# Kernel optimization log

Hardware: AMD Instinct MI355X
Metric: run time of the kernel (lower is better)

Reference implementation:

```python
import jax, jax.numpy as jnp
import numpy as np


def setup_inputs() -> dict:
    key = jax.random.key(0)
    pred = jax.random.normal(key, (16, 4, 768, 768), dtype=jnp.float32)
    return {"pred": pred}


def _largest_cc(mask):
    """Largest 4-connected component of a 2D boolean mask, as float32 0/1.

    Equivalent to scipy.ndimage.label (default 4-connectivity) followed by
    keeping the largest label. Uses min-label flood propagation: each
    foreground pixel starts with its raster index; iterated neighbor-min
    converges so every pixel holds its component's minimum pixel index
    (the 'root'). Ties in size resolve to the smallest root, which matches
    scipy's label-order tie-breaking (labels assigned in raster order).
    """
    H, W = mask.shape
    HW = H * W
    idx = jnp.arange(HW, dtype=jnp.int32).reshape(H, W)
    BIG = jnp.int32(HW)  # sentinel for background
    lbl0 = jnp.where(mask, idx, BIG)

    def body(carry):
        lbl, _ = carry
        p = jnp.pad(lbl, 1, constant_values=HW)
        nb = jnp.minimum(jnp.minimum(p[:-2, 1:-1], p[2:, 1:-1]),
                         jnp.minimum(p[1:-1, :-2], p[1:-1, 2:]))
        new = jnp.where(mask, jnp.minimum(lbl, nb), BIG)
        return new, jnp.any(new != lbl)

    lbl, _ = jax.lax.while_loop(lambda c: c[1], body, (lbl0, jnp.any(mask)))

    # component sizes keyed by root pixel index; background bucket = HW
    sizes = jax.ops.segment_sum(mask.ravel().astype(jnp.int32), lbl.ravel(),
                                num_segments=HW + 1)
    sizes = sizes.at[HW].set(0)
    root = jnp.argmax(sizes).astype(jnp.int32)
    return ((lbl == root) & mask).astype(jnp.float32)


def reference(pred):
    B, C, H, W = pred.shape
    labels = jnp.argmax(pred, axis=1)  # [B, H, W]
    cls = jnp.arange(1, C, dtype=labels.dtype)
    masks = labels[:, None, :, :] == cls[None, :, None, None]  # [B, C-1, H, W]
    comp = jax.vmap(_largest_cc)(masks.reshape(-1, H, W)).reshape(B, C - 1, H, W)
    bg = 1.0 - jnp.clip(comp.sum(axis=1), 0.0, 1.0)  # channel 0
    return jnp.concatenate([bg[:, None], comp], axis=1)
```

## Files before the change

### kernel.cpp

```cpp
#include <hip/hip_runtime.h>
#include <stdint.h>

#define BB 16
#define CC 4
#define HH 768
#define WW 768
#define HW (HH * WW)
#define NPIX (BB * HW)
#define NIMG (BB * (CC - 1))
#define BEST_STRIDE 16

#define SH 16
#define SW 64
#define SPIX (SH * SW)
#define SX (WW / SW)
#define SY (HH / SH)
#define SPI (SX * SY)
#define WPB 4
#define CCL_TPB (WPB * 64)

typedef unsigned long long ull;


__device__ __forceinline__ int find_root(int* P, int i) {
    int p = P[i];
    while (p != i) {
        int gp = P[p];
        P[i] = gp;
        i = p;
        p = gp;
    }
    return i;
}

__device__ __forceinline__ void merge(int* P, int a, int b) {
    a = find_root(P, a);
    b = find_root(P, b);
    while (a != b) {
        if (a < b) { int t = a; a = b; b = t; }
        int old = atomicCAS(&P[a], a, b);
        if (old == a) return;
        a = find_root(P, old);
        b = find_root(P, b);
    }
}


__device__ __forceinline__ int lfind(int* P, int i) {
    int p = P[i];
    while (p != i) {
        int gp = P[p];
        P[i] = gp;
        i = p;
        p = gp;
    }
    return i;
}

__device__ __forceinline__ void lmerge(int* P, int a, int b) {
    a = lfind(P, a);
    b = lfind(P, b);
    while (a != b) {
        if (a < b) { int t = a; a = b; b = t; }
        int old = atomicCAS(&P[a], a, b);
        if (old == a) return;
        a = lfind(P, old);
        b = lfind(P, b);
    }
}

__device__ __forceinline__ ull umax64(ull a, ull b) { return a > b ? a : b; }

__device__ __forceinline__ void lds_fence() {
    asm volatile("s_waitcnt lgkmcnt(0)" ::: "memory");
    __builtin_amdgcn_sched_barrier(0);
}


__global__ __launch_bounds__(CCL_TPB) void k_strip_ccl(
        const float* __restrict__ pred,
        uint8_t* __restrict__ labels,
        int* __restrict__ parent,
        uint32_t* __restrict__ counts,
        ull* __restrict__ best) {
    __shared__ __align__(16) int sp_all[WPB][SPIX];
    __shared__ __align__(16) uint8_t slab_all[WPB][SPIX];

    if (blockIdx.x == 0) {
        for (int i = threadIdx.x; i < NIMG * BEST_STRIDE; i += CCL_TPB) best[i] = 0ull;
    }

    const int tid = (int)threadIdx.x;
    const int w = tid >> 6;
    const int lane = tid & 63;
    int* sp = sp_all[w];
    uint8_t* slab = slab_all[w];

    const int gs = blockIdx.x * WPB + w;
    const int img = gs / SPI;
    const int s = gs % SPI;
    const int tr = (s / SX) * SH;
    const int tc = (s % SX) * SW;
    const float* pb = pred + (size_t)img * CC * HW;
    const int imgbase = img * HW;

    for (int it = 0; it < 4; ++it) {
        int li = it * 256 + lane * 4;
        int gi = (tr + (li >> 6)) * WW + tc + (li & 63);
        float4 v0 = *(const float4*)&pb[gi];
        float4 v1 = *(const float4*)&pb[gi + HW];
        float4 v2 = *(const float4*)&pb[gi + 2 * HW];
        float4 v3 = *(const float4*)&pb[gi + 3 * HW];
        const float* a0 = &v0.x; const float* a1 = &v1.x;
        const float* a2 = &v2.x; const float* a3 = &v3.x;
        uchar4 lout;
        uint8_t* lj = &lout.x;
        #pragma unroll
        for (int j = 0; j < 4; ++j) {
            int lab = 0;
            float bv = a0[j];
            if (a1[j] > bv) { bv = a1[j]; lab = 1; }
            if (a2[j] > bv) { bv = a2[j]; lab = 2; }
            if (a3[j] > bv) { bv = a3[j]; lab = 3; }
            lj[j] = (uint8_t)lab;
        }
        *(uchar4*)&slab[li] = lout;
        *(uchar4*)&labels[imgbase + gi] = lout;
    }
    lds_fence();

    {
        int prevLab = 0, prevV = 0;
        #pragma unroll 1
        for (int r = 0; r < SH; ++r) {
            int li = (r << 6) + lane;
            int lab = slab[li];
            int labL = __shfl_up(lab, 1, 64);
            bool isStart = lab && (lane == 0 || labL != lab);
            ull mask = __ballot(isStart);
            int v = li;
            if (lab) {
                ull mle = mask & (~0ull >> (63 - lane));
                v = (r << 6) + (63 - __clzll(mle));
            }
            sp[li] = v;
            lds_fence();
            int labUL = __shfl_up(prevLab, 1, 64);
            if (r > 0 && lab && prevLab == lab) {
                if (lane == 0 || !(labL == lab && labUL == lab))
                    lmerge(sp, v, prevV);
            }
            prevLab = lab;
            prevV = v;
        }
    }
    lds_fence();

    #pragma unroll 1
    for (int r = 0; r < SH; ++r) {
        int li = (r << 6) + lane;
        int lab = slab[li];
        int labL = __shfl_up(lab, 1, 64);
        bool isStart = lab && (lane == 0 || labL != lab);
        bool isEnd = lab && (lane == 63 || (int)slab[li + 1] != lab);
        ull endmask = __ballot(isEnd);
        if (lab) {
            int p = sp[li] & 0xFFFF;
            if (p != li) {
                int q0 = sp[p] & 0xFFFF;
                while (q0 != p) { p = q0; q0 = sp[p] & 0xFFFF; }
                sp[li] = p;
            }
            if (isStart) {
                ull mge = endmask & (~0ull << lane);
                int epos = __ffsll((long long)mge) - 1;
                int runlen = epos - lane + 1;
                atomicAdd((unsigned int*)&sp[p], (unsigned int)runlen << 16);
            }
        }
    }
    lds_fence();

    for (int it = 0; it < 4; ++it) {
        int li = it * 256 + lane * 4;
        int gi = imgbase + (tr + (li >> 6)) * WW + tc + (li & 63);
        uchar4 lv = *(const uchar4*)&slab[li];
        int4 sv = *(const int4*)&sp[li];
        const uint8_t* lj = &lv.x;
        const int* sj = &sv.x;
        int4 pout; uint4 cout;
        int* pj = &pout.x; uint32_t* cj = &cout.x;
        #pragma unroll
        for (int j = 0; j < 4; ++j) {
            int root = sj[j] & 0xFFFF;
            if (lj[j]) {
                pj[j] = imgbase + (tr + (root >> 6)) * WW + tc + (root & 63);
                cj[j] = (root == li + j) ? ((uint32_t)sj[j] >> 16) : 0u;
            } else {
                pj[j] = -1;
                cj[j] = 0u;
            }
        }
        *(int4*)&parent[gi] = pout;
        *(uint4*)&counts[gi] = cout;
    }
}

#define VED ((SX - 1) * HH)
#define HED ((SY - 1) * WW)
#define EPI (VED + HED)
__global__ void k_border_merge(const uint8_t* __restrict__ labels, int* parent) {
    int t = blockIdx.x * blockDim.x + threadIdx.x;
    if (t >= BB * EPI) return;
    int img = t / EPI;
    int e = t % EPI;
    int a, b;
    if (e < VED) {
        int j = e / HH, r = e % HH;
        int c = (j + 1) * SW - 1;
        a = r * WW + c;
        b = a + 1;
    } else {
        e -= VED;
        int j = e / WW, c = e % WW;
        int r = (j + 1) * SH - 1;
        a = r * WW + c;
        b = a + WW;
    }
    int ga = img * HW + a, gb = img * HW + b;
    uint8_t la = labels[ga];
    if (la && labels[gb] == la) merge(parent, ga, gb);
}

__global__ void k_compress(int* __restrict__ parent, uint32_t* __restrict__ counts) {
    int q = blockIdx.x * blockDim.x + threadIdx.x;
    if (q >= NPIX / 4) return;
    int t = q * 4;
    uint4 cv = *(const uint4*)&counts[t];
    if (!(cv.x | cv.y | cv.z | cv.w)) return;
    uint32_t cs[4] = {cv.x, cv.y, cv.z, cv.w};
    #pragma unroll
    for (int j = 0; j < 4; ++j) {
        if (!cs[j]) continue;
        int i = t + j;
        int g = parent[i];
        if (g == i) continue;
        while (true) { int pg = parent[g]; if (pg == g) break; g = pg; }
        parent[i] = g;
        atomicAdd(&counts[g], cs[j]);
        counts[i] = 0;
    }
}

#define BEST_BLK_PER_IMG 144
#define BEST_TPB 256
#define BEST_PIX_PER_BLK (HW / BEST_BLK_PER_IMG)
__global__ void k_best(const uint8_t* __restrict__ labels,
                       const uint32_t* __restrict__ counts,
                       ull* __restrict__ best) {
    __shared__ ull sw[(BEST_TPB / 64) * 3];
    int img = blockIdx.x / BEST_BLK_PER_IMG;
    int chunk = blockIdx.x % BEST_BLK_PER_IMG;
    int base = img * HW + chunk * BEST_PIX_PER_BLK;

    ull l0 = 0, l1 = 0, l2 = 0;
    for (int k = 0; k < BEST_PIX_PER_BLK; k += BEST_TPB * 4) {
        int t = base + k + (int)threadIdx.x * 4;
        uint4 cv = *(const uint4*)&counts[t];
        if (cv.x | cv.y | cv.z | cv.w) {
            uchar4 lv = *(const uchar4*)&labels[t];
            uint32_t cs[4] = {cv.x, cv.y, cv.z, cv.w};
            uint8_t ls[4] = {lv.x, lv.y, lv.z, lv.w};
            #pragma unroll
            for (int j = 0; j < 4; ++j) {
                if (cs[j]) {
                    int cc = (int)ls[j] - 1;
                    ull key = ((ull)cs[j] << 32) | (ull)(~(uint32_t)(t + j));
                    if (cc == 0) l0 = umax64(l0, key);
                    else if (cc == 1) l1 = umax64(l1, key);
                    else l2 = umax64(l2, key);
                }
            }
        }
    }
    #pragma unroll
    for (int m = 1; m < 64; m <<= 1) {
        l0 = umax64(l0, __shfl_xor(l0, m, 64));
        l1 = umax64(l1, __shfl_xor(l1, m, 64));
        l2 = umax64(l2, __shfl_xor(l2, m, 64));
    }
    int lane = threadIdx.x & 63;
    int wid = threadIdx.x >> 6;
    if (lane == 0) { sw[wid * 3 + 0] = l0; sw[wid * 3 + 1] = l1; sw[wid * 3 + 2] = l2; }
    __syncthreads();
    if (threadIdx.x < 3) {
        ull m = 0;
        for (int w = 0; w < BEST_TPB / 64; ++w) m = umax64(m, sw[w * 3 + threadIdx.x]);
        if (m) atomicMax(&best[(img * 3 + (int)threadIdx.x) * BEST_STRIDE], m);
    }
}

__global__ void k_output(const uint8_t* __restrict__ labels,
                         const int* __restrict__ parent,
                         const ull* __restrict__ best,
                         float* __restrict__ out) {
    int q = blockIdx.x * blockDim.x + threadIdx.x;
    if (q >= NPIX / 4) return;
    int t = q * 4;
    int b = t / HW;
    int i = t - b * HW;
    uchar4 lv = *(const uchar4*)&labels[t];
    int4 pv = *(const int4*)&parent[t];
    int root[3];
    root[0] = (int)(~(uint32_t)best[(b * 3 + 0) * BEST_STRIDE]);
    root[1] = (int)(~(uint32_t)best[(b * 3 + 1) * BEST_STRIDE]);
    root[2] = (int)(~(uint32_t)best[(b * 3 + 2) * BEST_STRIDE]);

    uint8_t ls[4] = {lv.x, lv.y, lv.z, lv.w};
    int ps[4] = {pv.x, pv.y, pv.z, pv.w};
    float fg[4];
    #pragma unroll
    for (int j = 0; j < 4; ++j) {
        int g = -1;
        if (ps[j] >= 0) g = parent[ps[j]];
        fg[j] = (ls[j] && g == root[ls[j] - 1]) ? 1.0f : 0.0f;
    }

    float4 o0, o1, o2, o3;
    float* c0 = &o0.x; float* c1 = &o1.x; float* c2 = &o2.x; float* c3 = &o3.x;
    #pragma unroll
    for (int j = 0; j < 4; ++j) {
        c0[j] = 1.0f - fg[j];
        c1[j] = (ls[j] == 1) ? fg[j] : 0.0f;
        c2[j] = (ls[j] == 2) ? fg[j] : 0.0f;
        c3[j] = (ls[j] == 3) ? fg[j] : 0.0f;
    }
    float* o = out + (size_t)b * CC * HW + i;
    *(float4*)&o[0] = o0;
    *(float4*)&o[HW] = o1;
    *(float4*)&o[2 * HW] = o2;
    *(float4*)&o[3 * HW] = o3;
}


extern "C" void kernel_launch(void* const* d_in, const int* in_sizes, int n_in,
                              void* d_out, int out_size, void* d_ws, size_t ws_size,
                              hipStream_t stream) {
    const float* pred = (const float*)d_in[0];
    float* out = (float*)d_out;

    uint8_t* labels = (uint8_t*)d_ws;
    int* parent = (int*)((char*)d_ws + NPIX);
    ull* best = (ull*)((char*)d_ws + NPIX + (size_t)NPIX * 4);
    uint32_t* counts = (uint32_t*)d_out;

    const int TPB = 256;

    k_strip_ccl<<<BB * SPI / WPB, CCL_TPB, 0, stream>>>(pred, labels, parent, counts, best);
    k_border_merge<<<(BB * EPI + TPB - 1) / TPB, TPB, 0, stream>>>(labels, parent);
    k_compress<<<(NPIX / 4 + TPB - 1) / TPB, TPB, 0, stream>>>(parent, counts);
    k_best<<<BB * BEST_BLK_PER_IMG, BEST_TPB, 0, stream>>>(labels, counts, best);
    k_output<<<(NPIX / 4 + TPB - 1) / TPB, TPB, 0, stream>>>(labels, parent, best, out);
}
```

Before: 155.9 us.

## Keep strip labels in registers and batch vertical merges after row pass

```diff
diff --git a/kernel.cpp b/kernel.cpp
--- a/kernel.cpp
+++ b/kernel.cpp
@@ -84,7 +84,6 @@
         uint32_t* __restrict__ counts,
         ull* __restrict__ best) {
     __shared__ __align__(16) int sp_all[WPB][SPIX];
-    __shared__ __align__(16) uint8_t slab_all[WPB][SPIX];
 
     if (blockIdx.x == 0) {
         for (int i = threadIdx.x; i < NIMG * BEST_STRIDE; i += CCL_TPB) best[i] = 0ull;
@@ -94,7 +93,6 @@
     const int w = tid >> 6;
     const int lane = tid & 63;
     int* sp = sp_all[w];
-    uint8_t* slab = slab_all[w];
 
     const int gs = blockIdx.x * WPB + w;
     const int img = gs / SPI;
@@ -103,68 +101,67 @@
     const int tc = (s % SX) * SW;
     const float* pb = pred + (size_t)img * CC * HW;
     const int imgbase = img * HW;
-
-    for (int it = 0; it < 4; ++it) {
-        int li = it * 256 + lane * 4;
-        int gi = (tr + (li >> 6)) * WW + tc + (li & 63);
-        float4 v0 = *(const float4*)&pb[gi];
-        float4 v1 = *(const float4*)&pb[gi + HW];
-        float4 v2 = *(const float4*)&pb[gi + 2 * HW];
-        float4 v3 = *(const float4*)&pb[gi + 3 * HW];
-        const float* a0 = &v0.x; const float* a1 = &v1.x;
-        const float* a2 = &v2.x; const float* a3 = &v3.x;
-        uchar4 lout;
-        uint8_t* lj = &lout.x;
-        #pragma unroll
-        for (int j = 0; j < 4; ++j) {
-            int lab = 0;
-            float bv = a0[j];
-            if (a1[j] > bv) { bv = a1[j]; lab = 1; }
-            if (a2[j] > bv) { bv = a2[j]; lab = 2; }
-            if (a3[j] > bv) { bv = a3[j]; lab = 3; }
-            lj[j] = (uint8_t)lab;
-        }
-        *(uchar4*)&slab[li] = lout;
-        *(uchar4*)&labels[imgbase + gi] = lout;
+    const int col0 = tr * WW + tc + lane;
+
+    int lab[SH];
+    int v[SH];
+
+    #pragma unroll
+    for (int r = 0; r < SH; ++r) {
+        int gi = col0 + r * WW;
+        float b0 = pb[gi];
+        float b1 = pb[gi + HW];
+        float b2 = pb[gi + 2 * HW];
+        float b3 = pb[gi + 3 * HW];
+        int l = 0;
+        float bv = b0;
+        if (b1 > bv) { bv = b1; l = 1; }
+        if (b2 > bv) { bv = b2; l = 2; }
+        if (b3 > bv) { bv = b3; l = 3; }
+        lab[r] = l;
+        labels[imgbase + gi] = (uint8_t)l;
+    }
+
+    #pragma unroll
+    for (int r = 0; r < SH; ++r) {
+        int l = lab[r];
+        int labL = __shfl_up(l, 1, 64);
+        bool isStart = l && (lane == 0 || labL != l);
+        ull mask = __ballot(isStart);
+        int li = (r << 6) + lane;
+        int vr = li;
+        if (l) {
+            ull mle = mask & (~0ull >> (63 - lane));
+            vr = (r << 6) + (63 - __clzll(mle));
+        }
+        v[r] = vr;
+        sp[li] = vr;
     }
     lds_fence();
 
-    {
-        int prevLab = 0, prevV = 0;
-        #pragma unroll 1
-        for (int r = 0; r < SH; ++r) {
-            int li = (r << 6) + lane;
-            int lab = slab[li];
-            int labL = __shfl_up(lab, 1, 64);
-            bool isStart = lab && (lane == 0 || labL != lab);
-            ull mask = __ballot(isStart);
-            int v = li;
-            if (lab) {
-                ull mle = mask & (~0ull >> (63 - lane));
-                v = (r << 6) + (63 - __clzll(mle));
-            }
-            sp[li] = v;
-            lds_fence();
-            int labUL = __shfl_up(prevLab, 1, 64);
-            if (r > 0 && lab && prevLab == lab) {
-                if (lane == 0 || !(labL == lab && labUL == lab))
-                    lmerge(sp, v, prevV);
-            }
-            prevLab = lab;
-            prevV = v;
+    #pragma unroll
+    for (int r = 1; r < SH; ++r) {
+        int l = lab[r];
+        int lU = lab[r - 1];
+        int labL = __shfl_up(l, 1, 64);
+        int labUL = __shfl_up(lU, 1, 64);
+        if (l && lU == l) {
+            if (lane == 0 || !(labL == l && labUL == l))
+                lmerge(sp, v[r], v[r - 1]);
         }
     }
     lds_fence();
 
-    #pragma unroll 1
+    #pragma unroll
     for (int r = 0; r < SH; ++r) {
+        int l = lab[r];
+        int labL = __shfl_up(l, 1, 64);
+        int labR = __shfl_down(l, 1, 64);
+        bool isStart = l && (lane == 0 || labL != l);
+        bool isEnd = l && (lane == 63 || labR != l);
+        ull endmask = __ballot(isEnd);
         int li = (r << 6) + lane;
-        int lab = slab[li];
-        int labL = __shfl_up(lab, 1, 64);
-        bool isStart = lab && (lane == 0 || labL != lab);
-        bool isEnd = lab && (lane == 63 || (int)slab[li + 1] != lab);
-        ull endmask = __ballot(isEnd);
-        if (lab) {
+        if (l) {
             int p = sp[li] & 0xFFFF;
             if (p != li) {
                 int q0 = sp[p] & 0xFFFF;
@@ -181,28 +178,20 @@
     }
     lds_fence();
 
-    for (int it = 0; it < 4; ++it) {
-        int li = it * 256 + lane * 4;
-        int gi = imgbase + (tr + (li >> 6)) * WW + tc + (li & 63);
-        uchar4 lv = *(const uchar4*)&slab[li];
-        int4 sv = *(const int4*)&sp[li];
-        const uint8_t* lj = &lv.x;
-        const int* sj = &sv.x;
-        int4 pout; uint4 cout;
-        int* pj = &pout.x; uint32_t* cj = &cout.x;
-        #pragma unroll
-        for (int j = 0; j < 4; ++j) {
-            int root = sj[j] & 0xFFFF;
-            if (lj[j]) {
-                pj[j] = imgbase + (tr + (root >> 6)) * WW + tc + (root & 63);
-                cj[j] = (root == li + j) ? ((uint32_t)sj[j] >> 16) : 0u;
-            } else {
-                pj[j] = -1;
-                cj[j] = 0u;
-            }
-        }
-        *(int4*)&parent[gi] = pout;
-        *(uint4*)&counts[gi] = cout;
+    #pragma unroll
+    for (int r = 0; r < SH; ++r) {
+        int li = (r << 6) + lane;
+        int gi = imgbase + col0 + r * WW;
+        int sv = sp[li];
+        int root = sv & 0xFFFF;
+        int pv = -1;
+        uint32_t cv = 0u;
+        if (lab[r]) {
+            pv = imgbase + (tr + (root >> 6)) * WW + tc + (root & 63);
+            cv = (root == li) ? ((uint32_t)sv >> 16) : 0u;
+        }
+        parent[gi] = pv;
+        counts[gi] = cv;
     }
 }
 
```

Result: no change. 154.7 us (-0.7%).
